# Kernel tuning notes

Hardware: AMD Instinct MI355X
Metric: run time of the kernel (lower is better)

The kernel has to match this reference:

```python
import jax, jax.numpy as jnp
import numpy as np

NUM_EMBEDDINGS = 8192
EMBEDDING_DIM = 256
COMMITMENT_COST = 0.25


def setup_inputs() -> dict:
    key = jax.random.key(0)
    kz, kw = jax.random.split(key)
    z = jax.random.normal(kz, (65536, EMBEDDING_DIM), dtype=jnp.float32)
    # nn.Embedding init: uniform(-1/K, 1/K)
    W = jax.random.uniform(kw, (NUM_EMBEDDINGS, EMBEDDING_DIM), dtype=jnp.float32,
                           minval=-1.0 / NUM_EMBEDDINGS, maxval=1.0 / NUM_EMBEDDINGS)
    return {"z": z, "W": W}


def reference(z, W):
    # distances[n, k] = ||z_n||^2 + ||W_k||^2 - 2 z_n . W_k  -> [N, K]
    distances = (jnp.sum(z * z, axis=1, keepdims=True)
                 + jnp.sum(W * W, axis=1)
                 - 2.0 * jnp.matmul(z, W.T))
    encoding_indices = jnp.argmin(distances, axis=1)  # [N]
    # one-hot @ W is just a gather of codebook rows
    quantized = W[encoding_indices]  # [N, D]
    e_latent_loss = jnp.mean((jax.lax.stop_gradient(quantized) - z) ** 2)
    q_latent_loss = jnp.mean((quantized - jax.lax.stop_gradient(z)) ** 2)
    loss = q_latent_loss + COMMITMENT_COST * e_latent_loss
    # straight-through estimator
    quantized_st = z + jax.lax.stop_gradient(quantized - z)
    return quantized_st, loss, encoding_indices[:, None]
```

## Files before the change

kernel.cpp:

```cpp
#include <hip/hip_runtime.h>

#define N_ROWS 65536
#define K_CODES 8192
#define DIM 256
#define CAP 56

#define LOSS_OFF (N_ROWS * DIM)
#define IDX_OFF (LOSS_OFF + 1)
#define OUT_WBF_U16 0
#define OUT_ZBF_U16 2097152
#define OUT_CAND_F 9437184

#define WS_LOSS 0
#define WS_ZNORM 64
#define WS_WNORM (WS_ZNORM + N_ROWS)
#define WS_MARGIN (WS_WNORM + K_CODES)
#define WS_CUT0 (WS_MARGIN + N_ROWS)
#define WS_CNT (WS_CUT0 + N_ROWS)
#define WS_OVF (WS_CNT + N_ROWS)
#define WS_OVFLIST (WS_OVF + 1)
#define WS_SLOT (((WS_OVFLIST + N_ROWS) + 1) & ~1)

typedef __bf16 bf16x8 __attribute__((ext_vector_type(8)));
typedef float f32x4 __attribute__((ext_vector_type(4)));


__device__ __forceinline__ float mul_rn_nofma(float a, float b) {
  float r;
  asm("v_mul_f32 %0, %1, %2" : "=v"(r) : "v"(a), "v"(b));
  return r;
}

__device__ __forceinline__ unsigned int f2bf(float f) {
  unsigned int u = __float_as_uint(f);
  return (u + 0x7FFFu + ((u >> 16) & 1u)) >> 16;
}

__device__ float dot_chain(const float* __restrict__ zp, const float* __restrict__ wp) {
  float acc = 0.0f;
#pragma unroll 8
  for (int d4 = 0; d4 < 64; ++d4) {
    const float4 a = *(const float4*)(zp + d4 * 4);
    const float4 b = *(const float4*)(wp + d4 * 4);
    acc = fmaf(a.x, b.x, acc);
    acc = fmaf(a.y, b.y, acc);
    acc = fmaf(a.z, b.z, acc);
    acc = fmaf(a.w, b.w, acc);
  }
  return acc;
}

__device__ __forceinline__ void glds16(const void* g, void* l) {
  __builtin_amdgcn_global_load_lds(
      (const __attribute__((address_space(1))) void*)(unsigned long long)(size_t)g,
      (__attribute__((address_space(3))) void*)(unsigned int)(size_t)l, 16, 0, 0);
}


__global__ void precvt_kernel(const float* __restrict__ z, const float* __restrict__ W,
                              unsigned short* __restrict__ outu) {
  const int t = blockIdx.x * blockDim.x + threadIdx.x;
  const int WQ = (K_CODES * DIM) / 4;
  const float4 v = (t < WQ) ? ((const float4*)W)[t] : ((const float4*)z)[t - WQ];
  uint2 p;
  p.x = f2bf(v.x) | (f2bf(v.y) << 16);
  p.y = f2bf(v.z) | (f2bf(v.w) << 16);
  ((uint2*)outu)[t] = p;
}

__global__ void norms_kernel(const float* __restrict__ z, const float* __restrict__ W,
                             float* __restrict__ ws) {
  const int tid = threadIdx.x;
  const int l = tid & 63, w = tid >> 6;
  const int j = l & 7, b = (l >> 3) & 1, rw = l >> 4;
  const int row = blockIdx.x * 16 + w * 4 + rw;
  const float* src = (row < N_ROWS) ? (z + (size_t)row * DIM + b * 128)
                                    : (W + (size_t)(row - N_ROWS) * DIM + b * 128);
  float a0 = src[j];
  float r = mul_rn_nofma(a0, a0);
  float s = fabsf(a0);
  for (int i = 8; i < 128; i += 8) {
    const float v = src[i + j];
    r = r + mul_rn_nofma(v, v);
    s = s + fabsf(v);
  }
  r = r + __shfl_xor(r, 1, 64);
  r = r + __shfl_xor(r, 2, 64);
  r = r + __shfl_xor(r, 4, 64);
  r = r + __shfl_xor(r, 8, 64);
  s = s + __shfl_xor(s, 1, 64);
  s = s + __shfl_xor(s, 2, 64);
  s = s + __shfl_xor(s, 4, 64);
  s = s + __shfl_xor(s, 8, 64);
  if ((l & 15) == 0) {
    if (row < N_ROWS) {
      ws[WS_ZNORM + row] = r;
      const float margin = 2.0e-6f * s + 4.0e-5f;
      ws[WS_MARGIN + row] = margin;
      ws[WS_CUT0 + row] = 3.10f * sqrtf(r) * 7.0467e-5f - margin;
      ((unsigned int*)ws)[WS_CNT + row] = 0u;
    } else {
      ws[WS_WNORM + (row - N_ROWS)] = r;
    }
  }
  if (blockIdx.x == 0 && tid == 0) {
    ws[WS_LOSS] = 0.0f;
    ((unsigned int*)ws)[WS_OVF] = 0u;
  }
}

__global__ __launch_bounds__(256) void gemm_screen_kernel(
    const unsigned short* __restrict__ zbf, const unsigned short* __restrict__ wbf,
    float* __restrict__ ws, uint2* __restrict__ candp) {
  __shared__ __align__(16) unsigned short As[128][64];
  __shared__ __align__(16) unsigned short Bs[128][64];
  __shared__ float cutbuf[128];

  const int tid = threadIdx.x;
  const int w = tid >> 6, l = tid & 63;
  const int lr = l & 15, lq = l >> 4;
  const int wr = (w >> 1) * 64, wc = (w & 1) * 64;
  const int rowBase = blockIdx.y * 128, colBase = blockIdx.x * 128;
  const int r8 = l >> 3, slot = l & 7;

  unsigned int* cntp = (unsigned int*)ws + WS_CNT;

  if (tid < 128) cutbuf[tid] = ws[WS_CUT0 + rowBase + tid];

  f32x4 acc[4][4];
#pragma unroll
  for (int mi = 0; mi < 4; ++mi)
#pragma unroll
    for (int ni = 0; ni < 4; ++ni) acc[mi][ni] = (f32x4){0.f, 0.f, 0.f, 0.f};

  for (int c = 0; c < 4; ++c) {
    __syncthreads();
    const int doff = c * 64;
#pragma unroll
    for (int j = 0; j < 4; ++j) {
      const int r_l = w * 32 + j * 8 + r8;
      const int ga = slot ^ (r_l & 7);
      glds16(zbf + (size_t)(rowBase + r_l) * DIM + doff + ga * 8, &As[w * 32 + j * 8][0]);
      glds16(wbf + (size_t)(colBase + r_l) * DIM + doff + ga * 8, &Bs[w * 32 + j * 8][0]);
    }
    __syncthreads();
#pragma unroll
    for (int kk = 0; kk < 2; ++kk) {
      const int g = kk * 4 + lq;
      bf16x8 af[4], bfr[4];
#pragma unroll
      for (int mi = 0; mi < 4; ++mi) {
        const int r_l = wr + mi * 16 + lr;
        af[mi] = *(const bf16x8*)&As[r_l][(g ^ (r_l & 7)) * 8];
      }
#pragma unroll
      for (int ni = 0; ni < 4; ++ni) {
        const int r_l = wc + ni * 16 + lr;
        bfr[ni] = *(const bf16x8*)&Bs[r_l][(g ^ (r_l & 7)) * 8];
      }
#pragma unroll
      for (int mi = 0; mi < 4; ++mi)
#pragma unroll
        for (int ni = 0; ni < 4; ++ni)
          acc[mi][ni] =
              __builtin_amdgcn_mfma_f32_16x16x32_bf16(af[mi], bfr[ni], acc[mi][ni], 0, 0, 0);
    }
  }

#pragma unroll
  for (int mi = 0; mi < 4; ++mi)
#pragma unroll
    for (int r = 0; r < 4; ++r) {
      const int lrow = wr + mi * 16 + lq * 4 + r;
      const float cut = cutbuf[lrow];
#pragma unroll
      for (int ni = 0; ni < 4; ++ni) {
        if (acc[mi][ni][r] >= cut) {
          const int grow = rowBase + lrow;
          const int gcol = colBase + wc + ni * 16 + lr;
          const unsigned int pos = atomicAdd(&cntp[grow], 1u);
          if (pos < CAP) {
            uint2 e;
            e.x = __float_as_uint(acc[mi][ni][r]);
            e.y = (unsigned int)gcol;
            candp[(size_t)grow * CAP + pos] = e;
          }
        }
      }
    }
}

__global__ void recheck_kernel(const float* __restrict__ z, const float* __restrict__ W,
                               float* __restrict__ ws, const uint2* __restrict__ candp,
                               float* __restrict__ out) {
  const int row = blockIdx.x * blockDim.x + threadIdx.x;
  const unsigned int cv = ((const unsigned int*)ws)[WS_CNT + row];
  const float margin = ws[WS_MARGIN + row];
  const float cut0 = ws[WS_CUT0 + row];
  bool fb = (cv == 0u) || (cv > CAP);
  float candmax = -3.4e38f;
  if (!fb) {
    for (unsigned int j = 0; j < cv; ++j)
      candmax = fmaxf(candmax, __uint_as_float(candp[(size_t)row * CAP + j].x));
    if (candmax - margin < cut0) fb = true;
  }
  if (fb) {
    ((unsigned long long*)((unsigned int*)ws + WS_SLOT))[row] = ~0ull;
    const unsigned int p = atomicAdd(&((unsigned int*)ws)[WS_OVF], 1u);
    ((unsigned int*)ws)[WS_OVFLIST + p] = (unsigned int)row;
    return;
  }
  const float fcut = candmax - margin;
  const float zn = ws[WS_ZNORM + row];
  const float* zp = z + (size_t)row * DIM;
  float best = 3.4e38f;
  int bi = K_CODES;
  for (unsigned int j = 0; j < cv; ++j) {
    const uint2 e = candp[(size_t)row * CAP + j];
    if (__uint_as_float(e.x) < fcut) continue;
    const int k = (int)e.y;
    const float m = dot_chain(zp, W + (size_t)k * DIM);
    const float dist = (zn + ws[WS_WNORM + k]) - 2.0f * m;
    if (dist < best || (dist == best && k < bi)) { best = dist; bi = k; }
  }
  out[IDX_OFF + row] = (float)bi;
}

__global__ void fallback_compute(const float* __restrict__ z, const float* __restrict__ W,
                                 float* __restrict__ ws) {
  __shared__ unsigned long long part[4];
  const unsigned int n = ((const unsigned int*)ws)[WS_OVF];
  unsigned long long* slots = (unsigned long long*)((unsigned int*)ws + WS_SLOT);
  const unsigned int total = n * 32u;
  for (unsigned int item = blockIdx.x; item < total; item += gridDim.x) {
    const int row = (int)((const unsigned int*)ws)[WS_OVFLIST + (item >> 5)];
    const int k = (int)(item & 31u) * 256 + threadIdx.x;
    const float zn = ws[WS_ZNORM + row];
    const float m = dot_chain(z + (size_t)row * DIM, W + (size_t)k * DIM);
    const float dist = (zn + ws[WS_WNORM + k]) - 2.0f * m;
    unsigned long long key =
        ((unsigned long long)__float_as_uint(dist) << 32) | (unsigned int)k;
#pragma unroll
    for (int s = 1; s < 64; s <<= 1) {
      const unsigned long long o = __shfl_xor((long long)key, s, 64);
      key = (o < key) ? o : key;
    }
    if ((threadIdx.x & 63) == 0) part[threadIdx.x >> 6] = key;
    __syncthreads();
    if (threadIdx.x == 0) {
      unsigned long long b = part[0];
      b = (part[1] < b) ? part[1] : b;
      b = (part[2] < b) ? part[2] : b;
      b = (part[3] < b) ? part[3] : b;
      atomicMin(&slots[row], b);
    }
    __syncthreads();
  }
}

__global__ void fallback_write(const float* __restrict__ ws, float* __restrict__ out) {
  const unsigned int i = blockIdx.x * blockDim.x + threadIdx.x;
  const unsigned int n = ((const unsigned int*)ws)[WS_OVF];
  if (i < n) {
    const int row = (int)((const unsigned int*)ws)[WS_OVFLIST + i];
    const unsigned long long key =
        ((const unsigned long long*)((const unsigned int*)ws + WS_SLOT))[row];
    out[IDX_OFF + row] = (float)(unsigned int)(key & 0xffffffffull);
  }
}

__global__ void gather_loss_kernel(const float* __restrict__ z, const float* __restrict__ W,
                                   float* __restrict__ out, float* __restrict__ ws) {
  const int tid = threadIdx.x;
  const int rowBase = blockIdx.x * 64;
  float lsum = 0.0f;
  for (int p = 0; p < 16; ++p) {
    const int row = rowBase + p * 4 + (tid >> 6);
    const int c4 = tid & 63;
    const int idx = (int)out[IDX_OFF + row];
    const float4 zv = *(const float4*)(z + (size_t)row * DIM + c4 * 4);
    const float4 qv = *(const float4*)(W + (size_t)idx * DIM + c4 * 4);
    float4 t, o;
    t.x = qv.x - zv.x; t.y = qv.y - zv.y; t.z = qv.z - zv.z; t.w = qv.w - zv.w;
    o.x = zv.x + t.x;  o.y = zv.y + t.y;  o.z = zv.z + t.z;  o.w = zv.w + t.w;
    *(float4*)(out + (size_t)row * DIM + c4 * 4) = o;
    lsum += t.x * t.x + t.y * t.y + t.z * t.z + t.w * t.w;
  }
#pragma unroll
  for (int m = 1; m < 64; m <<= 1) lsum += __shfl_xor(lsum, m, 64);
  __shared__ float part[4];
  if ((tid & 63) == 0) part[tid >> 6] = lsum;
  __syncthreads();
  if (tid == 0) atomicAdd(&ws[WS_LOSS], (part[0] + part[1]) + (part[2] + part[3]));
}

__global__ void finalize_kernel(const float* __restrict__ ws, float* __restrict__ out) {
  if (threadIdx.x == 0 && blockIdx.x == 0) {
    const float mean = ws[WS_LOSS] / (float)(N_ROWS * DIM);
    out[LOSS_OFF] = mean + 0.25f * mean;
  }
}

extern "C" void kernel_launch(void* const* d_in, const int* in_sizes, int n_in,
                              void* d_out, int out_size, void* d_ws, size_t ws_size,
                              hipStream_t stream) {
  (void)in_sizes; (void)n_in; (void)out_size; (void)ws_size;
  const float* z = (const float*)d_in[0];
  const float* W = (const float*)d_in[1];
  float* out = (float*)d_out;
  float* ws = (float*)d_ws;
  unsigned short* outu = (unsigned short*)d_out;
  const unsigned short* wbf = outu + OUT_WBF_U16;
  const unsigned short* zbf = outu + OUT_ZBF_U16;
  uint2* candp = (uint2*)((float*)d_out + OUT_CAND_F);

  hipLaunchKernelGGL(precvt_kernel, dim3(18432), dim3(256), 0, stream, z, W, outu);
  hipLaunchKernelGGL(norms_kernel, dim3((N_ROWS + K_CODES) / 16), dim3(256), 0, stream,
                     z, W, ws);
  hipLaunchKernelGGL(gemm_screen_kernel, dim3(K_CODES / 128, N_ROWS / 128), dim3(256),
                     0, stream, zbf, wbf, ws, candp);
  hipLaunchKernelGGL(recheck_kernel, dim3(N_ROWS / 256), dim3(256), 0, stream,
                     z, W, ws, candp, out);
  hipLaunchKernelGGL(fallback_compute, dim3(2048), dim3(256), 0, stream, z, W, ws);
  hipLaunchKernelGGL(fallback_write, dim3(256), dim3(256), 0, stream, ws, out);
  hipLaunchKernelGGL(gather_loss_kernel, dim3(N_ROWS / 64), dim3(256), 0, stream,
                     z, W, out, ws);
  hipLaunchKernelGGL(finalize_kernel, dim3(1), dim3(64), 0, stream, ws, out);
}
```

Measured before the change: 1.001 ms.

## Double-buffer GEMM K-chunks and parallelize candidate recheck per wavefront

The screening GEMM now uses two smaller shared-memory buffers of 32-wide K slices. The next slice is loaded while the current one is computed, which removes one barrier per step and overlaps global-to-LDS loads with MFMA work. The recheck kernel now gives one wavefront per row instead of one thread per row. Each lane evaluates one candidate's fp32 dot product, and shuffle reductions find the max and argmin. This removes serial per-thread loops over up to 56 candidates, at the cost of idle lanes when rows have few candidates.

```diff
diff --git a/kernel.cpp b/kernel.cpp
--- a/kernel.cpp
+++ b/kernel.cpp
@@ -112,8 +112,8 @@
 __global__ __launch_bounds__(256) void gemm_screen_kernel(
     const unsigned short* __restrict__ zbf, const unsigned short* __restrict__ wbf,
     float* __restrict__ ws, uint2* __restrict__ candp) {
-  __shared__ __align__(16) unsigned short As[128][64];
-  __shared__ __align__(16) unsigned short Bs[128][64];
+  __shared__ __align__(16) unsigned short As[2][128][32];
+  __shared__ __align__(16) unsigned short Bs[2][128][32];
   __shared__ float cutbuf[128];
 
   const int tid = threadIdx.x;
@@ -121,7 +121,7 @@
   const int lr = l & 15, lq = l >> 4;
   const int wr = (w >> 1) * 64, wc = (w & 1) * 64;
   const int rowBase = blockIdx.y * 128, colBase = blockIdx.x * 128;
-  const int r8 = l >> 3, slot = l & 7;
+  const int r16 = l >> 2, slot = l & 3;
 
   unsigned int* cntp = (unsigned int*)ws + WS_CNT;
 
@@ -133,38 +133,45 @@
 #pragma unroll
     for (int ni = 0; ni < 4; ++ni) acc[mi][ni] = (f32x4){0.f, 0.f, 0.f, 0.f};
 
-  for (int c = 0; c < 4; ++c) {
+  auto STAGE = [&](int c, int b) {
+#pragma unroll
+    for (int j = 0; j < 2; ++j) {
+      const int r_l = w * 32 + j * 16 + r16;
+      const int ga = slot ^ (r_l & 3);
+      glds16(zbf + (size_t)(rowBase + r_l) * DIM + c * 32 + ga * 8,
+             &As[b][w * 32 + j * 16][0]);
+      glds16(wbf + (size_t)(colBase + r_l) * DIM + c * 32 + ga * 8,
+             &Bs[b][w * 32 + j * 16][0]);
+    }
+  };
+
+  auto COMPUTE = [&](int b) {
+    bf16x8 af[4], bfr[4];
+#pragma unroll
+    for (int mi = 0; mi < 4; ++mi) {
+      const int r_l = wr + mi * 16 + lr;
+      af[mi] = *(const bf16x8*)&As[b][r_l][(lq ^ (r_l & 3)) * 8];
+    }
+#pragma unroll
+    for (int ni = 0; ni < 4; ++ni) {
+      const int r_l = wc + ni * 16 + lr;
+      bfr[ni] = *(const bf16x8*)&Bs[b][r_l][(lq ^ (r_l & 3)) * 8];
+    }
+#pragma unroll
+    for (int mi = 0; mi < 4; ++mi)
+#pragma unroll
+      for (int ni = 0; ni < 4; ++ni)
+        acc[mi][ni] =
+            __builtin_amdgcn_mfma_f32_16x16x32_bf16(af[mi], bfr[ni], acc[mi][ni], 0, 0, 0);
+  };
+
+  STAGE(0, 0);
+  __syncthreads();
+#pragma unroll
+  for (int c = 0; c < 8; ++c) {
+    if (c < 7) STAGE(c + 1, (c + 1) & 1);
+    COMPUTE(c & 1);
     __syncthreads();
-    const int doff = c * 64;
-#pragma unroll
-    for (int j = 0; j < 4; ++j) {
-      const int r_l = w * 32 + j * 8 + r8;
-      const int ga = slot ^ (r_l & 7);
-      glds16(zbf + (size_t)(rowBase + r_l) * DIM + doff + ga * 8, &As[w * 32 + j * 8][0]);
-      glds16(wbf + (size_t)(colBase + r_l) * DIM + doff + ga * 8, &Bs[w * 32 + j * 8][0]);
-    }
-    __syncthreads();
-#pragma unroll
-    for (int kk = 0; kk < 2; ++kk) {
-      const int g = kk * 4 + lq;
-      bf16x8 af[4], bfr[4];
-#pragma unroll
-      for (int mi = 0; mi < 4; ++mi) {
-        const int r_l = wr + mi * 16 + lr;
-        af[mi] = *(const bf16x8*)&As[r_l][(g ^ (r_l & 7)) * 8];
-      }
-#pragma unroll
-      for (int ni = 0; ni < 4; ++ni) {
-        const int r_l = wc + ni * 16 + lr;
-        bfr[ni] = *(const bf16x8*)&Bs[r_l][(g ^ (r_l & 7)) * 8];
-      }
-#pragma unroll
-      for (int mi = 0; mi < 4; ++mi)
-#pragma unroll
-        for (int ni = 0; ni < 4; ++ni)
-          acc[mi][ni] =
-              __builtin_amdgcn_mfma_f32_16x16x32_bf16(af[mi], bfr[ni], acc[mi][ni], 0, 0, 0);
-    }
   }
 
 #pragma unroll
@@ -193,37 +200,46 @@
 __global__ void recheck_kernel(const float* __restrict__ z, const float* __restrict__ W,
                                float* __restrict__ ws, const uint2* __restrict__ candp,
                                float* __restrict__ out) {
-  const int row = blockIdx.x * blockDim.x + threadIdx.x;
+  const int lane = threadIdx.x & 63;
+  const int row = blockIdx.x * 4 + (threadIdx.x >> 6);
   const unsigned int cv = ((const unsigned int*)ws)[WS_CNT + row];
   const float margin = ws[WS_MARGIN + row];
   const float cut0 = ws[WS_CUT0 + row];
   bool fb = (cv == 0u) || (cv > CAP);
-  float candmax = -3.4e38f;
-  if (!fb) {
-    for (unsigned int j = 0; j < cv; ++j)
-      candmax = fmaxf(candmax, __uint_as_float(candp[(size_t)row * CAP + j].x));
-    if (candmax - margin < cut0) fb = true;
-  }
+  uint2 e;
+  e.x = 0u; e.y = 0u;
+  float av = -3.4e38f;
+  if (!fb && lane < (int)cv) {
+    e = candp[(size_t)row * CAP + lane];
+    av = __uint_as_float(e.x);
+  }
+  float candmax = av;
+#pragma unroll
+  for (int s = 1; s < 64; s <<= 1) candmax = fmaxf(candmax, __shfl_xor(candmax, s, 64));
+  if (!fb && candmax - margin < cut0) fb = true;
   if (fb) {
-    ((unsigned long long*)((unsigned int*)ws + WS_SLOT))[row] = ~0ull;
-    const unsigned int p = atomicAdd(&((unsigned int*)ws)[WS_OVF], 1u);
-    ((unsigned int*)ws)[WS_OVFLIST + p] = (unsigned int)row;
+    if (lane == 0) {
+      ((unsigned long long*)((unsigned int*)ws + WS_SLOT))[row] = ~0ull;
+      const unsigned int p = atomicAdd(&((unsigned int*)ws)[WS_OVF], 1u);
+      ((unsigned int*)ws)[WS_OVFLIST + p] = (unsigned int)row;
+    }
     return;
   }
   const float fcut = candmax - margin;
-  const float zn = ws[WS_ZNORM + row];
-  const float* zp = z + (size_t)row * DIM;
-  float best = 3.4e38f;
-  int bi = K_CODES;
-  for (unsigned int j = 0; j < cv; ++j) {
-    const uint2 e = candp[(size_t)row * CAP + j];
-    if (__uint_as_float(e.x) < fcut) continue;
+  unsigned long long key = ~0ull;
+  if (lane < (int)cv && av >= fcut) {
     const int k = (int)e.y;
-    const float m = dot_chain(zp, W + (size_t)k * DIM);
+    const float zn = ws[WS_ZNORM + row];
+    const float m = dot_chain(z + (size_t)row * DIM, W + (size_t)k * DIM);
     const float dist = (zn + ws[WS_WNORM + k]) - 2.0f * m;
-    if (dist < best || (dist == best && k < bi)) { best = dist; bi = k; }
-  }
-  out[IDX_OFF + row] = (float)bi;
+    key = ((unsigned long long)__float_as_uint(dist) << 32) | (unsigned int)k;
+  }
+#pragma unroll
+  for (int s = 1; s < 64; s <<= 1) {
+    const unsigned long long o = (unsigned long long)__shfl_xor((long long)key, s, 64);
+    key = (o < key) ? o : key;
+  }
+  if (lane == 0) out[IDX_OFF + row] = (float)(unsigned int)(key & 0xffffffffull);
 }
 
 __global__ void fallback_compute(const float* __restrict__ z, const float* __restrict__ W,
@@ -319,7 +335,7 @@
                      z, W, ws);
   hipLaunchKernelGGL(gemm_screen_kernel, dim3(K_CODES / 128, N_ROWS / 128), dim3(256),
                      0, stream, zbf, wbf, ws, candp);
-  hipLaunchKernelGGL(recheck_kernel, dim3(N_ROWS / 256), dim3(256), 0, stream,
+  hipLaunchKernelGGL(recheck_kernel, dim3(N_ROWS / 4), dim3(256), 0, stream,
                      z, W, ws, candp, out);
   hipLaunchKernelGGL(fallback_compute, dim3(2048), dim3(256), 0, stream, z, W, ws);
   hipLaunchKernelGGL(fallback_write, dim3(256), dim3(256), 0, stream, ws, out);
```

Result: no change. 994.4 us (-0.6%).
